# Kernel tuning notes

Hardware: AMD Instinct MI355X
Metric: run time of the kernel (lower is better)

Reference implementation:

```python
import jax, jax.numpy as jnp
import numpy as np

B, S, D = 4, 2048, 768
H = 12
HD = D // H  # 64
EPS = 1e-12  # F.normalize eps


def setup_inputs() -> dict:
    key = jax.random.key(0)
    ks = jax.random.split(key, 6)
    scale = 1.0 / np.sqrt(D)
    x = jax.random.normal(ks[0], (B, S, D), dtype=jnp.float32)
    Wq = jax.random.normal(ks[1], (D, D), dtype=jnp.float32) * scale
    Wk = jax.random.normal(ks[2], (D, D), dtype=jnp.float32) * scale
    Wv = jax.random.normal(ks[3], (D, D), dtype=jnp.float32) * scale
    Wo = jax.random.normal(ks[4], (D, D), dtype=jnp.float32) * scale
    temperature = jnp.ones((H, 1, 1), dtype=jnp.float32)
    return {"x": x, "Wq": Wq, "Wk": Wk, "Wv": Wv, "Wo": Wo, "temperature": temperature}


def _heads(t):
    # [B,S,D] -> [B,H,S,HD]
    return t.reshape(B, S, H, HD).transpose(0, 2, 1, 3)


def reference(x, Wq, Wk, Wv, Wo, temperature):
    # Linear weights stored torch-style [out,in]: y = x @ W.T
    q = _heads(x @ Wq.T)
    k = _heads(x @ Wk.T)
    v = _heads(x @ Wv.T)
    # cosine-sim normalize (F.normalize: x / max(||x||, eps))
    q = q / jnp.maximum(jnp.linalg.norm(q, axis=-1, keepdims=True), EPS)
    k = k / jnp.maximum(jnp.linalg.norm(k, axis=-1, keepdims=True), EPS)
    # [B,H,S,S] scores with per-head learnable temperature
    attn = jnp.einsum("bhqd,bhkd->bhqk", q, k) * temperature  # temperature broadcasts [H,1,1]
    causal = jnp.tril(jnp.ones((S, S), dtype=bool))
    attn = jnp.where(causal, attn, -jnp.inf)
    attn = jax.nn.softmax(attn, axis=-1)
    out = jnp.einsum("bhqk,bhkd->bhqd", attn, v)
    out = out.transpose(0, 2, 1, 3).reshape(B, S, D)
    return out @ Wo.T
```

## Files before the change

### kernel.cpp

```cpp
#include <hip/hip_runtime.h>
#include <hip/hip_bf16.h>

#define B_ 4
#define S_ 2048
#define D_ 768
#define H_ 12
#define HD_ 64
#define M_ (B_*S_)
#define LOG2E 1.44269504088896f

typedef __attribute__((ext_vector_type(8))) short bf8;
typedef __attribute__((ext_vector_type(4))) float f4;
typedef unsigned short u16;
typedef unsigned int   u32;

typedef __attribute__((address_space(3))) u32 lds_u32;
typedef __attribute__((address_space(1))) const u32 glob_u32;

__device__ __forceinline__ float bf2f(u16 u) {
  union { u32 i; float f; } c; c.i = ((u32)u) << 16; return c.f;
}
__device__ __forceinline__ u16 f2bf(float x) {
  union { float f; u32 i; } c; c.f = x;
  u32 r = (c.i + 0x7FFFu + ((c.i >> 16) & 1u)) >> 16;
  return (u16)r;
}
__device__ __forceinline__ u16 cvt_bf16(float x) {
  u32 r;
  asm("v_cvt_pk_bf16_f32 %0, %1, %1" : "=v"(r) : "v"(x));
  return (u16)r;
}
__device__ __forceinline__ u32 cvt_pk2(float lo, float hi) {
  u32 r;
  asm("v_cvt_pk_bf16_f32 %0, %1, %2" : "=v"(r) : "v"(lo), "v"(hi));
  return r;
}
__device__ __forceinline__ float exp2_raw(float x) {
  float r;
  asm("v_exp_f32 %0, %1" : "=v"(r) : "v"(x));
  return r;
}
__device__ __forceinline__ void glds16(const u16* g, u16* l) {
  __builtin_amdgcn_global_load_lds((glob_u32*)g, (lds_u32*)l, 16, 0, 0);
}

__global__ __launch_bounds__(256) void stage_all(const float* __restrict__ x,
                                                 const float* __restrict__ w0, const float* __restrict__ w1,
                                                 const float* __restrict__ w2, const float* __restrict__ w3,
                                                 u16* __restrict__ xo,
                                                 u16* __restrict__ o0, u16* __restrict__ o1,
                                                 u16* __restrict__ o2, u16* __restrict__ o3,
                                                 int nx4, int nw4)
{
  int y = blockIdx.y;
  const float* src = (y == 0) ? x : (y == 1) ? w0 : (y == 2) ? w1 : (y == 3) ? w2 : w3;
  u16*         dst = (y == 0) ? xo : (y == 1) ? o0 : (y == 2) ? o1 : (y == 3) ? o2 : o3;
  int n4 = (y == 0) ? nx4 : nw4;
  for (int i = blockIdx.x * blockDim.x + threadIdx.x; i < n4; i += gridDim.x * blockDim.x) {
    float4 v = ((const float4*)src)[i];
    ushort4 o;
    o.x = f2bf(v.x); o.y = f2bf(v.y); o.z = f2bf(v.z); o.w = f2bf(v.w);
    ((ushort4*)dst)[i] = o;
  }
}

__global__ __launch_bounds__(256) void stage_cvt(const float* __restrict__ in,
                                                 u16* __restrict__ out, int n4)
{
  for (int i = blockIdx.x * blockDim.x + threadIdx.x; i < n4; i += gridDim.x * blockDim.x) {
    float4 v = ((const float4*)in)[i];
    ushort4 o;
    o.x = f2bf(v.x); o.y = f2bf(v.y); o.z = f2bf(v.z); o.w = f2bf(v.w);
    ((ushort4*)out)[i] = o;
  }
}

__device__ __forceinline__ bf8 ldcvt8(const float* __restrict__ p) {
  float4 a = *(const float4*)p;
  float4 b = *(const float4*)(p + 4);
  bf8 r;
  r[0] = f2bf(a.x); r[1] = f2bf(a.y); r[2] = f2bf(a.z); r[3] = f2bf(a.w);
  r[4] = f2bf(b.x); r[5] = f2bf(b.y); r[6] = f2bf(b.z); r[7] = f2bf(b.w);
  return r;
}

#define MFMA_BF16 __builtin_amdgcn_mfma_f32_16x16x32_bf16

template <int EPI>
__device__ __forceinline__ void gemm_core(u16* lds, int row0, int col0,
                                          const u16* __restrict__ A,
                                          const u16* __restrict__ W,
                                          u16* __restrict__ Cb,
                                          float* __restrict__ Cf,
                                          const float* __restrict__ temp)
{
  u16* a_lds = lds;
  u16* b_lds = lds + 64 * 64;

  const int w  = threadIdx.x >> 6;
  const int ln = threadIdx.x & 63;
  const int li = ln & 15, g = ln >> 4;
  const int wr = w >> 1, wc = w & 1;

  const int srow = ln >> 3;
  const int scol = ((ln & 7) ^ srow) * 8;
  const u16* Abase = A + (size_t)(row0 + srow) * 768 + scol;
  const u16* Bbase = W + (size_t)(col0 + srow) * 768 + scol;

  f4 acc[2][4];
#pragma unroll
  for (int i = 0; i < 2; ++i)
#pragma unroll
    for (int j = 0; j < 4; ++j) acc[i][j] = (f4){0.f, 0.f, 0.f, 0.f};

  for (int kt = 0; kt < 12; ++kt) {
    const int k0 = kt * 64;
#pragma unroll
    for (int i = 0; i < 2; ++i) {
      int seg = w * 2 + i;
      glds16(Abase + (size_t)(seg * 8) * 768 + k0, a_lds + seg * 512);
    }
#pragma unroll
    for (int i = 0; i < 4; ++i) {
      int seg = w * 4 + i;
      glds16(Bbase + (size_t)(seg * 8) * 768 + k0, b_lds + seg * 512);
    }
    asm volatile("s_waitcnt vmcnt(0)" ::: "memory");
    __syncthreads();

#pragma unroll
    for (int kk = 0; kk < 2; ++kk) {
      const int co = (((kk * 4 + g) ^ (li & 7)) * 8);
      bf8 a0 = *(const bf8*)(a_lds + (wr * 32 + li) * 64 + co);
      bf8 a1 = *(const bf8*)(a_lds + (wr * 32 + 16 + li) * 64 + co);
      bf8 b0 = *(const bf8*)(b_lds + (wc * 64 + li) * 64 + co);
      bf8 b1 = *(const bf8*)(b_lds + (wc * 64 + 16 + li) * 64 + co);
      bf8 b2 = *(const bf8*)(b_lds + (wc * 64 + 32 + li) * 64 + co);
      bf8 b3 = *(const bf8*)(b_lds + (wc * 64 + 48 + li) * 64 + co);
      acc[0][0] = MFMA_BF16(a0, b0, acc[0][0], 0, 0, 0);
      acc[0][1] = MFMA_BF16(a0, b1, acc[0][1], 0, 0, 0);
      acc[0][2] = MFMA_BF16(a0, b2, acc[0][2], 0, 0, 0);
      acc[0][3] = MFMA_BF16(a0, b3, acc[0][3], 0, 0, 0);
      acc[1][0] = MFMA_BF16(a1, b0, acc[1][0], 0, 0, 0);
      acc[1][1] = MFMA_BF16(a1, b1, acc[1][1], 0, 0, 0);
      acc[1][2] = MFMA_BF16(a1, b2, acc[1][2], 0, 0, 0);
      acc[1][3] = MFMA_BF16(a1, b3, acc[1][3], 0, 0, 0);
    }
    __syncthreads();
  }

  const int wrow0 = row0 + wr * 32;
  const int wcol0 = col0 + wc * 64;

  if (EPI == 1 || EPI == 2) {
    float tmul = 1.0f;
    if (EPI == 2) tmul = temp[wcol0 >> 6] * LOG2E;
#pragma unroll
    for (int i = 0; i < 2; ++i)
#pragma unroll
      for (int r = 0; r < 4; ++r) {
        float ss = 0.f;
#pragma unroll
        for (int j = 0; j < 4; ++j) ss += acc[i][j][r] * acc[i][j][r];
#pragma unroll
        for (int msk = 1; msk < 16; msk <<= 1) ss += __shfl_xor(ss, msk, 64);
        float scl = tmul / fmaxf(sqrtf(ss), 1e-12f);
#pragma unroll
        for (int j = 0; j < 4; ++j) acc[i][j][r] *= scl;
      }
  }

  if (EPI == 4) {
    __syncthreads();
#pragma unroll
    for (int i = 0; i < 2; ++i)
#pragma unroll
      for (int j = 0; j < 4; ++j)
#pragma unroll
        for (int r = 0; r < 4; ++r) {
          int cl = wc * 64 + j * 16 + li;
          int rl = wr * 32 + i * 16 + g * 4 + r;
          lds[cl * 64 + rl] = cvt_bf16(acc[i][j][r]);
        }
    __syncthreads();
    const int sb = row0 & 2047;
    const int bb = row0 >> 11;
#pragma unroll
    for (int q = 0; q < 4; ++q) {
      int c2 = threadIdx.x * 4 + q;
      int cl = c2 >> 3;
      int s8 = (c2 & 7) * 8;
      int colg = col0 + cl;
      int bh = bb * H_ + (colg >> 6);
      int d  = colg & 63;
      *(bf8*)(Cb + ((size_t)bh * 64 + d) * 2048 + sb + s8) = *(const bf8*)&lds[cl * 64 + s8];
    }
    return;
  }

#pragma unroll
  for (int i = 0; i < 2; ++i)
#pragma unroll
    for (int j = 0; j < 4; ++j)
#pragma unroll
      for (int r = 0; r < 4; ++r) {
        int row = wrow0 + i * 16 + g * 4 + r;
        int col = wcol0 + j * 16 + li;
        if (EPI == 3) Cf[(size_t)row * 768 + col] = acc[i][j][r];
        else          Cb[(size_t)row * 768 + col] = f2bf(acc[i][j][r]);
      }
}

__global__ __launch_bounds__(256) void gemm_qkv(const u16* __restrict__ XB,
                                                const u16* __restrict__ Wq, const u16* __restrict__ Wk,
                                                const u16* __restrict__ Wv,
                                                u16* __restrict__ Qb, u16* __restrict__ Kb,
                                                u16* __restrict__ Vt,
                                                const float* __restrict__ temp)
{
  __shared__ __align__(16) u16 lds[192 * 64];
  const int bid  = blockIdx.x;
  const int xcd  = bid & 7;
  const int j    = bid >> 3;
  const int row0 = (xcd * 16 + j / 18) * 64;
  const int rest = j % 18;
  const int z    = rest / 6;
  const int col0 = (rest % 6) * 128;
  if (z == 0)      gemm_core<2>(lds, row0, col0, XB, Wq, Qb, nullptr, temp);
  else if (z == 1) gemm_core<1>(lds, row0, col0, XB, Wk, Kb, nullptr, temp);
  else             gemm_core<4>(lds, row0, col0, XB, Wv, Vt, nullptr, temp);
}

__global__ __launch_bounds__(256) void gemm_out(const u16* __restrict__ A,
                                                const u16* __restrict__ W,
                                                float* __restrict__ Cf)
{
  __shared__ __align__(16) u16 lds[192 * 64];
  const int bid  = blockIdx.x;
  const int xcd  = bid & 7;
  const int j    = bid >> 3;
  const int row0 = (xcd * 16 + j / 6) * 64;
  const int col0 = (j % 6) * 128;
  gemm_core<3>(lds, row0, col0, A, W, nullptr, Cf, nullptr);
}

template <int EPI>
__global__ __launch_bounds__(256) void gemm_wf32(const u16* __restrict__ A,
                                                 const float* __restrict__ W,
                                                 u16* __restrict__ Cb,
                                                 float* __restrict__ Cf,
                                                 const float* __restrict__ temp)
{
  const int w  = threadIdx.x >> 6;
  const int ln = threadIdx.x & 63;
  const int li = ln & 15, g = ln >> 4;
  const int wr = w >> 1, wc = w & 1;
  const int row0 = blockIdx.x * 64 + wr * 32;
  const int col0 = blockIdx.y * 128 + wc * 64;

  const u16*   Ap = A + (size_t)(row0 + li) * 768 + g * 8;
  const float* Wp = W + (size_t)(col0 + li) * 768 + g * 8;

  f4 acc[2][4];
#pragma unroll
  for (int i = 0; i < 2; ++i)
#pragma unroll
    for (int j = 0; j < 4; ++j) acc[i][j] = (f4){0.f, 0.f, 0.f, 0.f};

  for (int k = 0; k < 768; k += 32) {
    bf8 a0 = *(const bf8*)(Ap + k);
    bf8 a1 = *(const bf8*)(Ap + (size_t)16 * 768 + k);
    bf8 b0 = ldcvt8(Wp + k);
    bf8 b1 = ldcvt8(Wp + (size_t)16 * 768 + k);
    bf8 b2 = ldcvt8(Wp + (size_t)32 * 768 + k);
    bf8 b3 = ldcvt8(Wp + (size_t)48 * 768 + k);
    acc[0][0] = MFMA_BF16(a0, b0, acc[0][0], 0, 0, 0);
    acc[0][1] = MFMA_BF16(a0, b1, acc[0][1], 0, 0, 0);
    acc[0][2] = MFMA_BF16(a0, b2, acc[0][2], 0, 0, 0);
    acc[0][3] = MFMA_BF16(a0, b3, acc[0][3], 0, 0, 0);
    acc[1][0] = MFMA_BF16(a1, b0, acc[1][0], 0, 0, 0);
    acc[1][1] = MFMA_BF16(a1, b1, acc[1][1], 0, 0, 0);
    acc[1][2] = MFMA_BF16(a1, b2, acc[1][2], 0, 0, 0);
    acc[1][3] = MFMA_BF16(a1, b3, acc[1][3], 0, 0, 0);
  }

  if (EPI == 1 || EPI == 2) {
    float tmul = 1.0f;
    if (EPI == 2) tmul = temp[col0 >> 6] * LOG2E;
#pragma unroll
    for (int i = 0; i < 2; ++i)
#pragma unroll
      for (int r = 0; r < 4; ++r) {
        float ss = 0.f;
#pragma unroll
        for (int j = 0; j < 4; ++j) ss += acc[i][j][r] * acc[i][j][r];
#pragma unroll
        for (int msk = 1; msk < 16; msk <<= 1) ss += __shfl_xor(ss, msk, 64);
        float scl = tmul / fmaxf(sqrtf(ss), 1e-12f);
#pragma unroll
        for (int j = 0; j < 4; ++j) acc[i][j][r] *= scl;
      }
  }

#pragma unroll
  for (int i = 0; i < 2; ++i)
#pragma unroll
    for (int j = 0; j < 4; ++j)
#pragma unroll
      for (int r = 0; r < 4; ++r) {
        int row = row0 + i * 16 + g * 4 + r;
        int col = col0 + j * 16 + li;
        if (EPI == 3)      Cf[(size_t)row * 768 + col] = acc[i][j][r];
        else if (EPI == 0) Cb[((size_t)((row >> 11) * H_ + (col >> 6)) * 64 + (col & 63)) * 2048
                              + (row & 2047)] = f2bf(acc[i][j][r]);
        else               Cb[(size_t)row * 768 + col] = f2bf(acc[i][j][r]);
      }
}

__global__ __launch_bounds__(256, 3) void flash_attn(const u16* __restrict__ Q,
                                                     const u16* __restrict__ K,
                                                     const u16* __restrict__ Vt,
                                                     u16* __restrict__ O,
                                                     const float* __restrict__ temp)
{
  const int bid = blockIdx.x;
  const int xcd = bid & 7;
  const int j   = bid >> 3;
  const int p_  = j & 31, rnd = j >> 5;
  const int pos = (rnd & 1) ? (31 - p_) : p_;
  const int rank = rnd * 32 + pos;
  const int qt  = 15 - rank / 6;
  const int bh  = xcd * 6 + rank % 6;
  const int b = bh / H_, h = bh % H_;
  const size_t base = (size_t)b * S_ * D_ + h * HD_;
  const u16* Qp  = Q + base;
  const u16* Kp  = K + base;
  const u16* Vtp = Vt + (size_t)bh * 64 * 2048;
  u16*       Op  = O + base;

  const float C2 = fabsf(temp[h]) * LOG2E;

  const int w  = threadIdx.x >> 6;
  const int ln = threadIdx.x & 63;
  const int li = ln & 15, g = ln >> 4;

  __shared__ __align__(16) u16 k_lds[64][72];
  __shared__ __align__(16) u16 vt[64][72];

  const int q0 = qt * 128;

  bf8 qf[2][2];
#pragma unroll
  for (int i = 0; i < 2; ++i) {
    const u16* qp = Qp + (size_t)(q0 + w * 32 + i * 16 + li) * D_;
    qf[i][0] = *(const bf8*)(qp + g * 8);
    qf[i][1] = *(const bf8*)(qp + 32 + g * 8);
  }

  const int r2 = (threadIdx.x >> 3) * 2;
  const int c0 = (threadIdx.x & 7) * 8;
  const u16* ksrc = Kp  + (size_t)r2 * D_ + c0;
  const u16* vsrc = Vtp + (size_t)r2 * 2048 + c0;

  bf8 ka = *(const bf8*)(ksrc);
  bf8 kb = *(const bf8*)(ksrc + D_);
  bf8 va = *(const bf8*)(vsrc);
  bf8 vb_ = *(const bf8*)(vsrc + 2048);

  f4 o[2][4];
  float lp[2] = {0.f, 0.f};
#pragma unroll
  for (int i = 0; i < 2; ++i)
#pragma unroll
    for (int c = 0; c < 4; ++c) o[i][c] = (f4){0.f, 0.f, 0.f, 0.f};

  const int addrA = (((g & 1) << 5) + li) << 2;
  const int addrB = addrA + 64;
  const int ghi   = g >> 1;

  const int nt = 2 * qt + 1;
  for (int kt = 0; kt <= nt; ++kt) {
    __syncthreads();
    {
      *(bf8*)&k_lds[r2][c0]     = ka;
      *(bf8*)&k_lds[r2 + 1][c0] = kb;
      *(bf8*)&vt[r2][c0]        = va;
      *(bf8*)&vt[r2 + 1][c0]    = vb_;
    }
    if (kt < nt) {
      const u16* ks = ksrc + (size_t)(kt + 1) * 64 * D_;
      const u16* vs = vsrc + (kt + 1) * 64;
      ka  = *(const bf8*)(ks);
      kb  = *(const bf8*)(ks + D_);
      va  = *(const bf8*)(vs);
      vb_ = *(const bf8*)(vs + 2048);
    }
    asm volatile("s_waitcnt lgkmcnt(0)" ::: "memory");
    __builtin_amdgcn_s_barrier();

    f4 sc[4][2];
#pragma unroll
    for (int kb2 = 0; kb2 < 4; ++kb2) {
      sc[kb2][0] = (f4){0.f, 0.f, 0.f, 0.f};
      sc[kb2][1] = (f4){0.f, 0.f, 0.f, 0.f};
      bf8 k0 = *(const bf8*)&k_lds[kb2 * 16 + li][g * 8];
      bf8 k1 = *(const bf8*)&k_lds[kb2 * 16 + li][32 + g * 8];
      sc[kb2][0] = MFMA_BF16(k0, qf[0][0], sc[kb2][0], 0, 0, 0);
      sc[kb2][0] = MFMA_BF16(k1, qf[0][1], sc[kb2][0], 0, 0, 0);
      sc[kb2][1] = MFMA_BF16(k0, qf[1][0], sc[kb2][1], 0, 0, 0);
      sc[kb2][1] = MFMA_BF16(k1, qf[1][1], sc[kb2][1], 0, 0, 0);
    }

    if (kt >= 2 * qt) {
#pragma unroll
      for (int kb2 = 0; kb2 < 4; ++kb2)
#pragma unroll
        for (int qb = 0; qb < 2; ++qb)
#pragma unroll
          for (int r = 0; r < 4; ++r) {
            int key  = kt * 64 + kb2 * 16 + g * 4 + r;
            int qrow = q0 + w * 32 + qb * 16 + li;
            if (key > qrow) sc[kb2][qb][r] = -__builtin_inff();
          }
    }

    u32 pkv[2][4][2];
#pragma unroll
    for (int qb = 0; qb < 2; ++qb)
#pragma unroll
      for (int kb2 = 0; kb2 < 4; ++kb2) {
        float p0 = exp2_raw(sc[kb2][qb][0] - C2);
        float p1 = exp2_raw(sc[kb2][qb][1] - C2);
        float p2 = exp2_raw(sc[kb2][qb][2] - C2);
        float p3 = exp2_raw(sc[kb2][qb][3] - C2);
        lp[qb] += (p0 + p1) + (p2 + p3);
        pkv[qb][kb2][0] = cvt_pk2(p0, p1);
        pkv[qb][kb2][1] = cvt_pk2(p2, p3);
      }

#pragma unroll
    for (int ks = 0; ks < 2; ++ks) {
#pragma unroll
      for (int qb = 0; qb < 2; ++qb) {
        int e = 2 * ks, o1 = 2 * ks + 1;
        u32 a0 = (u32)__builtin_amdgcn_ds_bpermute(addrA, (int)pkv[qb][e][0]);
        u32 b0 = (u32)__builtin_amdgcn_ds_bpermute(addrA, (int)pkv[qb][o1][0]);
        u32 a1 = (u32)__builtin_amdgcn_ds_bpermute(addrA, (int)pkv[qb][e][1]);
        u32 b1 = (u32)__builtin_amdgcn_ds_bpermute(addrA, (int)pkv[qb][o1][1]);
        u32 a2 = (u32)__builtin_amdgcn_ds_bpermute(addrB, (int)pkv[qb][e][0]);
        u32 b2 = (u32)__builtin_amdgcn_ds_bpermute(addrB, (int)pkv[qb][o1][0]);
        u32 a3 = (u32)__builtin_amdgcn_ds_bpermute(addrB, (int)pkv[qb][e][1]);
        u32 b3 = (u32)__builtin_amdgcn_ds_bpermute(addrB, (int)pkv[qb][o1][1]);
        union { u32 u[4]; bf8 v; } pa;
        pa.u[0] = ghi ? b0 : a0;
        pa.u[1] = ghi ? b1 : a1;
        pa.u[2] = ghi ? b2 : a2;
        pa.u[3] = ghi ? b3 : a3;
#pragma unroll
        for (int c = 0; c < 4; ++c) {
          bf8 vv = *(const bf8*)&vt[c * 16 + li][ks * 32 + g * 8];
          o[qb][c] = MFMA_BF16(pa.v, vv, o[qb][c], 0, 0, 0);
        }
      }
    }
  }

  float linv[2][4];
#pragma unroll
  for (int qb = 0; qb < 2; ++qb) {
    float t = lp[qb];
    t += __shfl_xor(t, 16, 64);
    t += __shfl_xor(t, 32, 64);
    union { float f; int i; } ci; ci.f = t;
#pragma unroll
    for (int r = 0; r < 4; ++r) {
      int src = (g * 4 + r) << 2;
      union { int i; float f; } cv;
      cv.i = __builtin_amdgcn_ds_bpermute(src, ci.i);
      linv[qb][r] = 1.0f / cv.f;
    }
  }
#pragma unroll
  for (int qb = 0; qb < 2; ++qb)
#pragma unroll
    for (int c = 0; c < 4; ++c)
#pragma unroll
      for (int r = 0; r < 4; ++r) {
        int row = q0 + w * 32 + qb * 16 + g * 4 + r;
        Op[(size_t)row * D_ + c * 16 + li] = cvt_bf16(o[qb][c][r] * linv[qb][r]);
      }
}

extern "C" void kernel_launch(void* const* d_in, const int* in_sizes, int n_in,
                              void* d_out, int out_size, void* d_ws, size_t ws_size,
                              hipStream_t stream) {
  const void *xv, *Wqv, *Wkv, *Wvv, *Wov, *tv;
  if (in_sizes[0] == M_ * D_) {
    xv = d_in[0]; Wqv = d_in[1]; Wkv = d_in[2]; Wvv = d_in[3]; Wov = d_in[4]; tv = d_in[5];
  } else {
    Wkv = d_in[0]; Wov = d_in[1]; Wqv = d_in[2]; Wvv = d_in[3]; tv = d_in[4]; xv = d_in[5];
  }
  const float* x    = (const float*)xv;
  const float* Wq   = (const float*)Wqv;
  const float* Wk   = (const float*)Wkv;
  const float* Wv   = (const float*)Wvv;
  const float* Wo   = (const float*)Wov;
  const float* temp = (const float*)tv;

  const size_t SZ  = (size_t)M_ * D_;
  const size_t WSZ = (size_t)D_ * D_;
  u16* ws = (u16*)d_ws;
  u16* Qb = ws;
  u16* Kb = ws + SZ;
  u16* Vt = ws + 2 * SZ;
  u16* XB = (u16*)d_out;

  const bool stageW = ws_size >= (3 * SZ + 4 * WSZ) * sizeof(u16);
  u16* Wqb = ws + 3 * SZ;
  u16* Wkb = Wqb + WSZ;
  u16* Wvb = Wkb + WSZ;
  u16* Wob = Wvb + WSZ;

  if (stageW) {
    stage_all<<<dim3(512, 5), 256, 0, stream>>>(x, Wq, Wk, Wv, Wo,
                                                XB, Wqb, Wkb, Wvb, Wob,
                                                (int)(SZ / 4), (int)(WSZ / 4));
    gemm_qkv<<<2304, 256, 0, stream>>>(XB, Wqb, Wkb, Wvb, Qb, Kb, Vt, temp);
    flash_attn<<<768, 256, 0, stream>>>(Qb, Kb, Vt, Qb, temp);
    gemm_out<<<768, 256, 0, stream>>>(Qb, Wob, (float*)d_out);
  } else {
    dim3 gg(M_ / 64, D_ / 128), bb(256);
    stage_cvt<<<2048, 256, 0, stream>>>(x, XB, (int)(SZ / 4));
    gemm_wf32<2><<<gg, bb, 0, stream>>>(XB, Wq, Qb, nullptr, temp);
    gemm_wf32<1><<<gg, bb, 0, stream>>>(XB, Wk, Kb, nullptr, temp);
    gemm_wf32<0><<<gg, bb, 0, stream>>>(XB, Wv, Vt, nullptr, temp);
    flash_attn<<<768, 256, 0, stream>>>(Qb, Kb, Vt, Qb, temp);
    gemm_wf32<3><<<gg, bb, 0, stream>>>(Qb, Wo, nullptr, (float*)d_out, temp);
  }
}
```

Before: 125.0 us.

## Fuse x fp32-to-bf16 conversion into QKV GEMM A-tile loading

```diff
diff --git a/kernel.cpp b/kernel.cpp
--- a/kernel.cpp
+++ b/kernel.cpp
@@ -43,19 +43,23 @@
 __device__ __forceinline__ void glds16(const u16* g, u16* l) {
   __builtin_amdgcn_global_load_lds((glob_u32*)g, (lds_u32*)l, 16, 0, 0);
 }
-
-__global__ __launch_bounds__(256) void stage_all(const float* __restrict__ x,
-                                                 const float* __restrict__ w0, const float* __restrict__ w1,
-                                                 const float* __restrict__ w2, const float* __restrict__ w3,
-                                                 u16* __restrict__ xo,
-                                                 u16* __restrict__ o0, u16* __restrict__ o1,
-                                                 u16* __restrict__ o2, u16* __restrict__ o3,
-                                                 int nx4, int nw4)
+__device__ __forceinline__ bf8 pack8(float4 a, float4 b) {
+  union { u32 u[4]; bf8 v; } r;
+  r.u[0] = cvt_pk2(a.x, a.y);
+  r.u[1] = cvt_pk2(a.z, a.w);
+  r.u[2] = cvt_pk2(b.x, b.y);
+  r.u[3] = cvt_pk2(b.z, b.w);
+  return r.v;
+}
+
+__global__ __launch_bounds__(256) void stage_w4(const float* __restrict__ w0, const float* __restrict__ w1,
+                                                const float* __restrict__ w2, const float* __restrict__ w3,
+                                                u16* __restrict__ o0, u16* __restrict__ o1,
+                                                u16* __restrict__ o2, u16* __restrict__ o3, int n4)
 {
   int y = blockIdx.y;
-  const float* src = (y == 0) ? x : (y == 1) ? w0 : (y == 2) ? w1 : (y == 3) ? w2 : w3;
-  u16*         dst = (y == 0) ? xo : (y == 1) ? o0 : (y == 2) ? o1 : (y == 3) ? o2 : o3;
-  int n4 = (y == 0) ? nx4 : nw4;
+  const float* src = (y == 0) ? w0 : (y == 1) ? w1 : (y == 2) ? w2 : w3;
+  u16*         dst = (y == 0) ? o0 : (y == 1) ? o1 : (y == 2) ? o2 : o3;
   for (int i = blockIdx.x * blockDim.x + threadIdx.x; i < n4; i += gridDim.x * blockDim.x) {
     float4 v = ((const float4*)src)[i];
     ushort4 o;
@@ -86,9 +90,10 @@
 
 #define MFMA_BF16 __builtin_amdgcn_mfma_f32_16x16x32_bf16
 
-template <int EPI>
+template <int EPI, int AF32>
 __device__ __forceinline__ void gemm_core(u16* lds, int row0, int col0,
-                                          const u16* __restrict__ A,
+                                          const u16* __restrict__ A16,
+                                          const float* __restrict__ A32,
                                           const u16* __restrict__ W,
                                           u16* __restrict__ Cb,
                                           float* __restrict__ Cf,
@@ -104,8 +109,22 @@
 
   const int srow = ln >> 3;
   const int scol = ((ln & 7) ^ srow) * 8;
-  const u16* Abase = A + (size_t)(row0 + srow) * 768 + scol;
   const u16* Bbase = W + (size_t)(col0 + srow) * 768 + scol;
+  const u16* Abase16 = AF32 ? nullptr : A16 + (size_t)(row0 + srow) * 768 + scol;
+
+  const int rA = threadIdx.x >> 2;
+  const int s0 = (threadIdx.x & 3) * 2;
+  const int c0g = (s0 ^ (rA & 7)) * 8;
+  const int c1g = ((s0 + 1) ^ (rA & 7)) * 8;
+  const float* Arow = AF32 ? A32 + (size_t)(row0 + rA) * 768 : nullptr;
+
+  float4 ar0a, ar0b, ar1a, ar1b;
+  if (AF32) {
+    ar0a = *(const float4*)(Arow + c0g);
+    ar0b = *(const float4*)(Arow + c0g + 4);
+    ar1a = *(const float4*)(Arow + c1g);
+    ar1b = *(const float4*)(Arow + c1g + 4);
+  }
 
   f4 acc[2][4];
 #pragma unroll
@@ -115,10 +134,16 @@
 
   for (int kt = 0; kt < 12; ++kt) {
     const int k0 = kt * 64;
-#pragma unroll
-    for (int i = 0; i < 2; ++i) {
-      int seg = w * 2 + i;
-      glds16(Abase + (size_t)(seg * 8) * 768 + k0, a_lds + seg * 512);
+    __syncthreads();
+    if (AF32) {
+      *(bf8*)(a_lds + rA * 64 + s0 * 8)       = pack8(ar0a, ar0b);
+      *(bf8*)(a_lds + rA * 64 + (s0 + 1) * 8) = pack8(ar1a, ar1b);
+    } else {
+#pragma unroll
+      for (int i = 0; i < 2; ++i) {
+        int seg = w * 2 + i;
+        glds16(Abase16 + (size_t)(seg * 8) * 768 + k0, a_lds + seg * 512);
+      }
     }
 #pragma unroll
     for (int i = 0; i < 4; ++i) {
@@ -126,7 +151,15 @@
       glds16(Bbase + (size_t)(seg * 8) * 768 + k0, b_lds + seg * 512);
     }
     asm volatile("s_waitcnt vmcnt(0)" ::: "memory");
-    __syncthreads();
+    asm volatile("s_waitcnt lgkmcnt(0)" ::: "memory");
+    __builtin_amdgcn_s_barrier();
+    if (AF32 && kt < 11) {
+      const float* an = Arow + (kt + 1) * 64;
+      ar0a = *(const float4*)(an + c0g);
+      ar0b = *(const float4*)(an + c0g + 4);
+      ar1a = *(const float4*)(an + c1g);
+      ar1b = *(const float4*)(an + c1g + 4);
+    }
 
 #pragma unroll
     for (int kk = 0; kk < 2; ++kk) {
@@ -146,7 +179,6 @@
       acc[1][2] = MFMA_BF16(a1, b2, acc[1][2], 0, 0, 0);
       acc[1][3] = MFMA_BF16(a1, b3, acc[1][3], 0, 0, 0);
     }
-    __syncthreads();
   }
 
   const int wrow0 = row0 + wr * 32;
@@ -211,7 +243,7 @@
       }
 }
 
-__global__ __launch_bounds__(256) void gemm_qkv(const u16* __restrict__ XB,
+__global__ __launch_bounds__(256) void gemm_qkv(const float* __restrict__ x,
                                                 const u16* __restrict__ Wq, const u16* __restrict__ Wk,
                                                 const u16* __restrict__ Wv,
                                                 u16* __restrict__ Qb, u16* __restrict__ Kb,
@@ -226,9 +258,9 @@
   const int rest = j % 18;
   const int z    = rest / 6;
   const int col0 = (rest % 6) * 128;
-  if (z == 0)      gemm_core<2>(lds, row0, col0, XB, Wq, Qb, nullptr, temp);
-  else if (z == 1) gemm_core<1>(lds, row0, col0, XB, Wk, Kb, nullptr, temp);
-  else             gemm_core<4>(lds, row0, col0, XB, Wv, Vt, nullptr, temp);
+  if (z == 0)      gemm_core<2, 1>(lds, row0, col0, nullptr, x, Wq, Qb, nullptr, temp);
+  else if (z == 1) gemm_core<1, 1>(lds, row0, col0, nullptr, x, Wk, Kb, nullptr, temp);
+  else             gemm_core<4, 1>(lds, row0, col0, nullptr, x, Wv, Vt, nullptr, temp);
 }
 
 __global__ __launch_bounds__(256) void gemm_out(const u16* __restrict__ A,
@@ -241,7 +273,7 @@
   const int j    = bid >> 3;
   const int row0 = (xcd * 16 + j / 6) * 64;
   const int col0 = (j % 6) * 128;
-  gemm_core<3>(lds, row0, col0, A, W, nullptr, Cf, nullptr);
+  gemm_core<3, 0>(lds, row0, col0, A, nullptr, W, nullptr, Cf, nullptr);
 }
 
 template <int EPI>
@@ -513,7 +545,6 @@
   u16* Qb = ws;
   u16* Kb = ws + SZ;
   u16* Vt = ws + 2 * SZ;
-  u16* XB = (u16*)d_out;
 
   const bool stageW = ws_size >= (3 * SZ + 4 * WSZ) * sizeof(u16);
   u16* Wqb = ws + 3 * SZ;
@@ -522,14 +553,14 @@
   u16* Wob = Wvb + WSZ;
 
   if (stageW) {
-    stage_all<<<dim3(512, 5), 256, 0, stream>>>(x, Wq, Wk, Wv, Wo,
-                                                XB, Wqb, Wkb, Wvb, Wob,
-                                                (int)(SZ / 4), (int)(WSZ / 4));
-    gemm_qkv<<<2304, 256, 0, stream>>>(XB, Wqb, Wkb, Wvb, Qb, Kb, Vt, temp);
+    stage_w4<<<dim3(192, 4), 256, 0, stream>>>(Wq, Wk, Wv, Wo,
+                                               Wqb, Wkb, Wvb, Wob, (int)(WSZ / 4));
+    gemm_qkv<<<2304, 256, 0, stream>>>(x, Wqb, Wkb, Wvb, Qb, Kb, Vt, temp);
     flash_attn<<<768, 256, 0, stream>>>(Qb, Kb, Vt, Qb, temp);
     gemm_out<<<768, 256, 0, stream>>>(Qb, Wob, (float*)d_out);
   } else {
     dim3 gg(M_ / 64, D_ / 128), bb(256);
+    u16* XB = (u16*)d_out;
     stage_cvt<<<2048, 256, 0, stream>>>(x, XB, (int)(SZ / 4));
     gemm_wf32<2><<<gg, bb, 0, stream>>>(XB, Wq, Qb, nullptr, temp);
     gemm_wf32<1><<<gg, bb, 0, stream>>>(XB, Wk, Kb, nullptr, temp);
```

Measured after the change: 136.3 us. 1.09x slower.
